# Performance work log

Hardware: AMD Instinct MI355X
Metric: run time of the kernel (lower is better)

The kernel has to match this reference:

```python
import jax, jax.numpy as jnp
import numpy as np

V, D, H, L, S, B = 32000, 512, 8, 6, 1024, 4
DH = D // H
T_ITERS = 2  # tree_iterations


def _ln(x, w, b, eps=1e-5):
    mu = jnp.mean(x, axis=-1, keepdims=True)
    var = jnp.mean((x - mu) ** 2, axis=-1, keepdims=True)
    return (x - mu) * jax.lax.rsqrt(var + eps) * w + b


def setup_inputs() -> dict:
    key = jax.random.key(0)
    ks = jax.random.split(key, 16)
    std = 0.02
    inp = {
        'input_ids': jax.random.randint(ks[0], (B, S), 0, V),
        'tok_emb': jax.random.normal(ks[1], (V, D), jnp.float32) * std,
        'pos_emb': jax.random.normal(ks[2], (S, D), jnp.float32) * std,
        # attention params, stacked over layers
        'Wq': jax.random.normal(ks[3], (L, D, D), jnp.float32) * std,
        'bq': jnp.zeros((L, D), jnp.float32),
        'Wk': jax.random.normal(ks[4], (L, D, D), jnp.float32) * std,
        'bk': jnp.zeros((L, D), jnp.float32),
        'Wv': jax.random.normal(ks[5], (L, D, D), jnp.float32) * std,
        'bv': jnp.zeros((L, D), jnp.float32),
        'Wo': jax.random.normal(ks[6], (L, D, D), jnp.float32) * std,
        'bo': jnp.zeros((L, D), jnp.float32),
        'ln1w': jnp.ones((L, D), jnp.float32), 'ln1b': jnp.zeros((L, D), jnp.float32),
        'ln2w': jnp.ones((L, D), jnp.float32), 'ln2b': jnp.zeros((L, D), jnp.float32),
        # TreeFFN params: input proj, edge proj (concat src,dst), gate
        'Win': jax.random.normal(ks[7], (L, D, D), jnp.float32) * std,
        'bin_': jnp.zeros((L, D), jnp.float32),
        'Wedge': jax.random.normal(ks[8], (L, 2 * D, D), jnp.float32) * std,
        'bedge': jnp.zeros((L, D), jnp.float32),
        'Wgate': jax.random.normal(ks[9], (L, D, D), jnp.float32) * std,
        'bgate': jnp.zeros((L, D), jnp.float32),
        'lnfw': jnp.ones((D,), jnp.float32), 'lnfb': jnp.zeros((D,), jnp.float32),
        'Whead': jax.random.normal(ks[10], (D, V), jnp.float32) * std,
    }
    return inp


def reference(input_ids, tok_emb, pos_emb, Wq, bq, Wk, bk, Wv, bv, Wo, bo,
              ln1w, ln1b, ln2w, ln2b, Win, bin_, Wedge, bedge, Wgate, bgate,
              lnfw, lnfb, Whead):
    b, s = input_ids.shape
    h = tok_emb[input_ids] + pos_emb[None, :s]  # [B,S,D]
    causal = jnp.tril(jnp.ones((s, s), bool))
    scale = 1.0 / jnp.sqrt(jnp.asarray(DH, h.dtype))
    for l in range(L):
        # --- multi-head self-attention with causal mask ---
        x = _ln(h, ln1w[l], ln1b[l])
        q = (x @ Wq[l] + bq[l]).reshape(b, s, H, DH)
        k = (x @ Wk[l] + bk[l]).reshape(b, s, H, DH)
        v = (x @ Wv[l] + bv[l]).reshape(b, s, H, DH)
        scores = jnp.einsum('bqhd,bkhd->bhqk', q, k) * scale
        scores = jnp.where(causal[None, None], scores, jnp.finfo(scores.dtype).min)
        attn = jax.nn.softmax(scores, axis=-1)
        av = jnp.einsum('bhqk,bkhd->bqhd', attn, v).reshape(b, s, D)
        h = h + av @ Wo[l] + bo[l]
        # --- TreeFFN: sequential-edge (i->i+1) message passing ---
        t = _ln(h, ln2w[l], ln2b[l]) @ Win[l] + bin_[l]
        for _ in range(T_ITERS):
            # edges: src = nodes 0..S-2, dst = nodes 1..S-1
            msg = jax.nn.relu(
                jnp.concatenate([t[:, :-1], t[:, 1:]], axis=-1) @ Wedge[l] + bedge[l]
            )  # [B,S-1,D]
            agg = jnp.pad(msg, ((0, 0), (1, 0), (0, 0)))  # scatter-add at dst nodes
            gate = jax.nn.sigmoid(agg @ Wgate[l] + bgate[l])
            t = t + gate * agg
        h = h + t
    h = _ln(h, lnfw, lnfb)
    return h @ Whead  # [B,S,V]
```

## Files before the change

### kernel.cpp

```cpp
#include <hip/hip_runtime.h>
#include <hip/hip_bf16.h>
#include <stdint.h>

#define V_ 32000
#define D_ 512
#define H_ 8
#define L_ 6
#define S_ 1024
#define B_ 4
#define DH_ 64
#define M_ (B_*S_)

typedef __attribute__((ext_vector_type(8))) short bf16x8;
typedef __attribute__((ext_vector_type(4))) short short4b;
typedef __attribute__((ext_vector_type(4))) float f32x4;

__device__ __forceinline__ short f2bs(float f) {
  union { float f; uint32_t u; } x; x.f = f;
  uint32_t r = (x.u + 0x7FFFu + ((x.u >> 16) & 1u)) >> 16;
  return (short)r;
}
__device__ __forceinline__ float bs2f(short s) {
  union { uint32_t u; float f; } x; x.u = ((uint32_t)(uint16_t)s) << 16;
  return x.f;
}

__device__ __forceinline__ f32x4 mfma16(bf16x8 a, bf16x8 b, f32x4 c) {
  return __builtin_amdgcn_mfma_f32_16x16x32_bf16(a, b, c, 0, 0, 0);
}

__device__ __forceinline__ void gload16(const short* g, char* lds) {
  __builtin_amdgcn_global_load_lds(
      (const __attribute__((address_space(1))) uint32_t*)g,
      (__attribute__((address_space(3))) uint32_t*)lds, 16, 0, 0);
}

template<int N> __device__ __forceinline__ void waitvm() {
  if constexpr (N == 0) asm volatile("s_waitcnt vmcnt(0)" ::: "memory");
  else if constexpr (N == 3) asm volatile("s_waitcnt vmcnt(3)" ::: "memory");
  else if constexpr (N == 4) asm volatile("s_waitcnt vmcnt(4)" ::: "memory");
  else if constexpr (N == 6) asm volatile("s_waitcnt vmcnt(6)" ::: "memory");
  else if constexpr (N == 8) asm volatile("s_waitcnt vmcnt(8)" ::: "memory");
}

__global__ __launch_bounds__(256) void transpose_cvt(const float* __restrict__ in,
    short* __restrict__ out, int K, int N, size_t in_slab, size_t out_slab, int orow0) {
  __shared__ float tile[32][33];
  const float* inp = in + (size_t)blockIdx.z * in_slab;
  short* outp = out + (size_t)blockIdx.z * out_slab;
  int kb = blockIdx.y * 32, nb = blockIdx.x * 32;
  int tx = threadIdx.x, ty = threadIdx.y;
  for (int r = ty; r < 32; r += 8) {
    int k = kb + r, n = nb + tx;
    tile[r][tx] = (k < K && n < N) ? inp[(size_t)k * N + n] : 0.f;
  }
  __syncthreads();
  for (int r = ty; r < 32; r += 8) {
    int n = nb + r, k = kb + tx;
    if (n < N && k < K) outp[(size_t)(orow0 + n) * K + k] = f2bs(tile[tx][r]);
  }
}

__global__ __launch_bounds__(256) void pack_qkv_bias(const float* __restrict__ bq,
    const float* __restrict__ bk, const float* __restrict__ bv, float* __restrict__ o) {
  int i = blockIdx.x * 256 + threadIdx.x;
  int l = i / 1536, c = i - l * 1536;
  float v = (c < 512) ? bq[l * 512 + c] : (c < 1024) ? bk[l * 512 + c - 512]
                                                     : bv[l * 512 + c - 1024];
  o[i] = v;
}

__global__ __launch_bounds__(256) void embed_k(const int* __restrict__ ids,
    const float* __restrict__ tok, const float* __restrict__ pos, float* __restrict__ h) {
  int bs = blockIdx.x;
  int tid = threadIdx.x;
  int s = bs & (S_ - 1);
  int id = ids[bs];
  float2 te = *(const float2*)(tok + (size_t)id * D_ + tid * 2);
  float2 pe = *(const float2*)(pos + (size_t)s * D_ + tid * 2);
  float2 r; r.x = te.x + pe.x; r.y = te.y + pe.y;
  *(float2*)(h + (size_t)bs * D_ + tid * 2) = r;
}

__global__ __launch_bounds__(256) void ln4_k(const float* __restrict__ in,
    const float* __restrict__ w, const float* __restrict__ bb, short* __restrict__ outb) {
  int wv = threadIdx.x >> 6, lane = threadIdx.x & 63;
  int row = blockIdx.x * 4 + wv;
  const float* x = in + (size_t)row * D_ + lane * 8;
  float4 v0 = *(const float4*)x;
  float4 v1 = *(const float4*)(x + 4);
  float s = v0.x + v0.y + v0.z + v0.w + v1.x + v1.y + v1.z + v1.w;
  #pragma unroll
  for (int o = 32; o; o >>= 1) s += __shfl_xor(s, o);
  float mu = s * (1.f / D_);
  float d[8] = {v0.x-mu, v0.y-mu, v0.z-mu, v0.w-mu, v1.x-mu, v1.y-mu, v1.z-mu, v1.w-mu};
  float s2 = 0.f;
  #pragma unroll
  for (int j = 0; j < 8; ++j) s2 += d[j] * d[j];
  #pragma unroll
  for (int o = 32; o; o >>= 1) s2 += __shfl_xor(s2, o);
  float rs = rsqrtf(s2 * (1.f / D_) + 1e-5f);
  float4 w0 = *(const float4*)(w + lane * 8);
  float4 w1 = *(const float4*)(w + lane * 8 + 4);
  float4 b0 = *(const float4*)(bb + lane * 8);
  float4 b1 = *(const float4*)(bb + lane * 8 + 4);
  float wj[8] = {w0.x,w0.y,w0.z,w0.w,w1.x,w1.y,w1.z,w1.w};
  float bj[8] = {b0.x,b0.y,b0.z,b0.w,b1.x,b1.y,b1.z,b1.w};
  short o8[8];
  #pragma unroll
  for (int j = 0; j < 8; ++j) o8[j] = f2bs(d[j] * rs * wj[j] + bj[j]);
  *(uint4*)(outb + (size_t)row * D_ + lane * 8) = *(uint4*)o8;
}

template<int AMODE, int EMODE, int BM, int BN>
__global__ __launch_bounds__(256) void gemm3_k(
    const short* __restrict__ A, const short* __restrict__ Wt,
    const float* __restrict__ bias, float* __restrict__ Cf,
    short* __restrict__ Cb, const short* __restrict__ Agg,
    float* __restrict__ Hf, const short* __restrict__ zpad,
    int M, int N, int K)
{
  constexpr int NF = BN / 32;
  constexpr int AR = BM / 32;
  constexpr int BR = BN / 32;
  constexpr int MI = BM / 32;
  constexpr int LOADS = AR + BR;
  __shared__ __align__(16) char As[2][BM * 128];
  __shared__ __align__(16) char Bs[2][BN * 128];
  const int tid = threadIdx.x;
  const int lane = tid & 63, w = tid >> 6;
  const int m0 = blockIdx.x * BM, n0 = blockIdx.y * BN;
  const int l15 = lane & 15, l4 = lane >> 4;
  const int wm = (w >> 1) * (BM / 2), wn = (w & 1) * (BN / 2);

  const int lrow_b = tid >> 3;
  const int kel0 = (tid & 7) * 8;
  const short* agp[AR];
  const short* agpHi[AR];
  #pragma unroll
  for (int r = 0; r < AR; ++r) {
    int lrow = r * 32 + lrow_b;
    int row = m0 + lrow;
    int kel = kel0 ^ ((lrow & 7) << 3);
    if (AMODE == 0) {
      agp[r] = A + (size_t)row * K + kel;
    } else if (AMODE == 1) {
      agp[r]   = A + (size_t)row * D_ + kel;
      agpHi[r] = ((row & (S_ - 1)) == (S_ - 1)) ? zpad + kel
                                                : A + (size_t)(row + 1) * D_ + kel;
    } else {
      agp[r] = ((row & (S_ - 1)) == 0) ? zpad + kel : A + (size_t)(row - 1) * D_ + kel;
    }
  }
  const short* bgp[BR];
  #pragma unroll
  for (int r = 0; r < BR; ++r) {
    int lrow = r * 32 + lrow_b;
    int kel = kel0 ^ ((lrow & 7) << 3);
    bgp[r] = Wt + (size_t)(n0 + lrow) * K + kel;
  }

  auto stage = [&](int buf, int k0) {
    #pragma unroll
    for (int r = 0; r < AR; ++r) {
      const short* gp;
      if (AMODE == 1) gp = (k0 < D_) ? agp[r] + k0 : agpHi[r] + (k0 - D_);
      else gp = agp[r] + k0;
      gload16(gp, As[buf] + r * 4096 + w * 1024);
    }
    #pragma unroll
    for (int r = 0; r < BR; ++r)
      gload16(bgp[r] + k0, Bs[buf] + r * 4096 + w * 1024);
  };

  const int rswz = (l15 & 7) << 4;
  int aoff[MI], boff[NF];
  #pragma unroll
  for (int i = 0; i < MI; ++i) aoff[i] = (wm + i * 16 + l15) * 128;
  #pragma unroll
  for (int j = 0; j < NF; ++j) boff[j] = (wn + j * 16 + l15) * 128;

  f32x4 acc[MI][NF] = {};

  const int nk = K >> 6;
  stage(0, 0);
  for (int t = 0; t < nk; ++t) {
    const int cur = t & 1;
    if (t + 1 < nk) { stage(cur ^ 1, (t + 1) * 64); waitvm<LOADS>(); }
    else waitvm<0>();
    __syncthreads();
    #pragma unroll
    for (int kk = 0; kk < 2; ++kk) {
      const int cb = (kk * 64 + l4 * 16) ^ rswz;
      bf16x8 af[MI], bfr[NF];
      #pragma unroll
      for (int i = 0; i < MI; ++i) af[i] = *(const bf16x8*)(As[cur] + aoff[i] + cb);
      #pragma unroll
      for (int j = 0; j < NF; ++j) bfr[j] = *(const bf16x8*)(Bs[cur] + boff[j] + cb);
      __builtin_amdgcn_s_setprio(1);
      #pragma unroll
      for (int i = 0; i < MI; ++i)
        #pragma unroll
        for (int j = 0; j < NF; ++j)
          acc[i][j] = mfma16(af[i], bfr[j], acc[i][j]);
      __builtin_amdgcn_s_setprio(0);
    }
    __syncthreads();
  }

  const int rowb = m0 + wm + l4 * 4;
  const int colb = n0 + wn + l15;
  #pragma unroll
  for (int i = 0; i < MI; ++i) {
    #pragma unroll
    for (int j = 0; j < NF; ++j) {
      int col = colb + j * 16;
      float bias_v = bias ? bias[col] : 0.f;
      #pragma unroll
      for (int r = 0; r < 4; ++r) {
        int row = rowb + i * 16 + r;
        size_t idx = (size_t)row * N + col;
        float v = acc[i][j][r] + bias_v;
        if (EMODE == 0) {
          if (Cb) { Cf[idx] = v; Cb[idx] = f2bs(v); }
          else __builtin_nontemporal_store(v, &Cf[idx]);
        } else if (EMODE == 1) {
          Cf[idx] += v;
        } else if (EMODE == 2) {
          Cb[idx] = f2bs(fmaxf(v, 0.f));
        } else if (EMODE == 3) {
          float g = 1.f / (1.f + __expf(-v));
          float aggv = ((row & (S_ - 1)) == 0) ? 0.f : bs2f(Agg[idx - N]);
          float tn = bs2f(Cb[idx]) + g * aggv;
          Cb[idx] = f2bs(tn);
        } else if (EMODE == 5) {
          float g = 1.f / (1.f + __expf(-v));
          float aggv = ((row & (S_ - 1)) == 0) ? 0.f : bs2f(Agg[idx - N]);
          Hf[idx] += bs2f(Cb[idx]) + g * aggv;
        } else if (EMODE == 6) {
          Cb[idx] = f2bs(v);
        } else {
          float sc = (col < D_) ? 0.180336880f : 1.f;
          Cb[idx] = f2bs(v * sc);
        }
      }
    }
  }
}

__global__ __launch_bounds__(256) void gemm2_k(
    const short* __restrict__ A, const short* __restrict__ Wt,
    float* __restrict__ Cf, int M, int N, int K)
{
  __shared__ __align__(16) char As[2][128 * 128];
  __shared__ __align__(16) char Bs[2][128 * 128];
  const int tid = threadIdx.x;
  const int lane = tid & 63, w = tid >> 6;
  const int nwg = gridDim.x * gridDim.y;
  const int bid = blockIdx.x + blockIdx.y * gridDim.x;
  const int swz = (bid & 7) * (nwg >> 3) + (bid >> 3);
  const int m0 = (swz % gridDim.x) * 128, n0 = (swz / gridDim.x) * 128;
  const int l15 = lane & 15, l4 = lane >> 4;
  const int wm = (w >> 1) * 64, wn = (w & 1) * 64;

  const int lrow_b = tid >> 3;
  const int kel0 = (tid & 7) * 8;
  const short* agp[4];
  const short* bgp[4];
  #pragma unroll
  for (int r = 0; r < 4; ++r) {
    int lrow = r * 32 + lrow_b;
    int kel = kel0 ^ ((lrow & 7) << 3);
    agp[r] = A + (size_t)(m0 + lrow) * K + kel;
    bgp[r] = Wt + (size_t)(n0 + lrow) * K + kel;
  }
  auto stage = [&](int buf, int k0) {
    #pragma unroll
    for (int r = 0; r < 4; ++r) gload16(agp[r] + k0, As[buf] + r * 4096 + w * 1024);
    #pragma unroll
    for (int r = 0; r < 4; ++r) gload16(bgp[r] + k0, Bs[buf] + r * 4096 + w * 1024);
  };

  const int rswz = (l15 & 7) << 4;
  int aoff[4], boff[4];
  #pragma unroll
  for (int i = 0; i < 4; ++i) aoff[i] = (wm + i * 16 + l15) * 128;
  #pragma unroll
  for (int j = 0; j < 4; ++j) boff[j] = (wn + j * 16 + l15) * 128;

  f32x4 acc[4][4] = {};
  const int nk = K >> 6;
  stage(0, 0);
  for (int t = 0; t < nk; ++t) {
    const int cur = t & 1;
    if (t + 1 < nk) { stage(cur ^ 1, (t + 1) * 64); waitvm<8>(); }
    else waitvm<0>();
    __syncthreads();
    #pragma unroll
    for (int kk = 0; kk < 2; ++kk) {
      const int cb = (kk * 64 + l4 * 16) ^ rswz;
      bf16x8 af[4], bfr[4];
      #pragma unroll
      for (int i = 0; i < 4; ++i) af[i] = *(const bf16x8*)(As[cur] + aoff[i] + cb);
      #pragma unroll
      for (int j = 0; j < 4; ++j) bfr[j] = *(const bf16x8*)(Bs[cur] + boff[j] + cb);
      __builtin_amdgcn_s_setprio(1);
      #pragma unroll
      for (int i = 0; i < 4; ++i)
        #pragma unroll
        for (int j = 0; j < 4; ++j)
          acc[i][j] = mfma16(af[i], bfr[j], acc[i][j]);
      __builtin_amdgcn_s_setprio(0);
    }
    __syncthreads();
  }

  const int rowb = m0 + wm + l4 * 4;
  const int colb = n0 + wn + l15;
  #pragma unroll
  for (int i = 0; i < 4; ++i)
    #pragma unroll
    for (int j = 0; j < 4; ++j)
      #pragma unroll
      for (int r = 0; r < 4; ++r) {
        size_t idx = (size_t)(rowb + i * 16 + r) * N + colb + j * 16;
        __builtin_nontemporal_store(acc[i][j][r], &Cf[idx]);
      }
}

__global__ __launch_bounds__(256) void fattn_k(const short* __restrict__ Qkv,
    short* __restrict__ avb)
{
  __shared__ short Ks[64][72];
  __shared__ short Vt[64][72];
  __shared__ short Pt[4][16][72];
  const int QS = 3 * D_;
  const int tid = threadIdx.x, lane = tid & 63, w = tid >> 6;
  const int bx = blockIdx.x;
  const int qt = 15 - (bx >> 5);
  const int bh = bx & 31, b = bh >> 3, hh = bh & 7;
  const int l15 = lane & 15, g = lane >> 4;

  const int qrow = qt * 64 + w * 16 + l15;
  const short* qptr = Qkv + (size_t)(b * S_ + qrow) * QS + hh * DH_;
  bf16x8 qa0 = *(const bf16x8*)(qptr + g * 8);
  bf16x8 qa1 = *(const bf16x8*)(qptr + 32 + g * 8);

  f32x4 o[4] = {};
  float mx = -1e30f, lsum = 0.f;

  auto gptr = [&](int kt, int i) {
    int c = tid + i * 256;
    int key = c >> 3, d0 = (c & 7) * 8;
    return Qkv + (size_t)(b * S_ + kt * 64 + key) * QS + hh * DH_ + d0;
  };
  uint4 kvA[2], vvA[2], kvB[2], vvB[2];
  auto load_t = [&](int kt, uint4 kv[2], uint4 vv[2]) {
    #pragma unroll
    for (int i = 0; i < 2; ++i) {
      const short* base = gptr(kt, i);
      kv[i] = *(const uint4*)(base + D_);
      vv[i] = *(const uint4*)(base + 2 * D_);
    }
  };
  auto store_t = [&](uint4 kv[2], uint4 vv[2]) {
    #pragma unroll
    for (int i = 0; i < 2; ++i) {
      int c = tid + i * 256;
      int key = c >> 3, d0 = (c & 7) * 8;
      *(uint4*)&Ks[key][d0] = kv[i];
      short vs[8]; *(uint4*)vs = vv[i];
      int a = (c & 7);
      #pragma unroll
      for (int j = 0; j < 8; ++j)
        Vt[d0 + j][key ^ (a << 3)] = vs[j];
    }
  };

  auto compute = [&](int kt) {
    const int key0 = kt * 64;
    f32x4 sc[4] = {};
    __builtin_amdgcn_s_setprio(1);
    #pragma unroll
    for (int f = 0; f < 4; ++f) {
      bf16x8 ka0 = *(const bf16x8*)&Ks[f * 16 + l15][g * 8];
      bf16x8 ka1 = *(const bf16x8*)&Ks[f * 16 + l15][32 + g * 8];
      sc[f] = mfma16(ka0, qa0, sc[f]);
      sc[f] = mfma16(ka1, qa1, sc[f]);
    }
    __builtin_amdgcn_s_setprio(0);

    float s[16];
    #pragma unroll
    for (int f = 0; f < 4; ++f)
      #pragma unroll
      for (int r = 0; r < 4; ++r)
        s[f * 4 + r] = sc[f][r];
    if (kt == qt) {
      #pragma unroll
      for (int f = 0; f < 4; ++f)
        #pragma unroll
        for (int r = 0; r < 4; ++r)
          if (key0 + f * 16 + g * 4 + r > qrow) s[f * 4 + r] = -1e30f;
    }
    float cm = s[0];
    #pragma unroll
    for (int i = 1; i < 16; ++i) cm = fmaxf(cm, s[i]);
    cm = fmaxf(cm, __shfl_xor(cm, 16));
    cm = fmaxf(cm, __shfl_xor(cm, 32));
    float mn = fmaxf(mx, cm);
    float fr = exp2f(mx - mn);
    mx = mn;
    float p[16], ss = 0.f;
    #pragma unroll
    for (int i = 0; i < 16; ++i) { p[i] = exp2f(s[i] - mn); ss += p[i]; }
    ss += __shfl_xor(ss, 16);
    ss += __shfl_xor(ss, 32);
    lsum = lsum * fr + ss;
    #pragma unroll
    for (int nt = 0; nt < 4; ++nt)
      #pragma unroll
      for (int r = 0; r < 4; ++r) o[nt][r] *= fr;

    #pragma unroll
    for (int f = 0; f < 4; ++f) {
      short tmp[4];
      #pragma unroll
      for (int r = 0; r < 4; ++r) tmp[r] = f2bs(p[f * 4 + r]);
      *(uint2*)&Pt[w][l15][f * 16 + g * 4] = *(uint2*)tmp;
    }
    __builtin_amdgcn_sched_barrier(0);
    bf16x8 pb0 = *(const bf16x8*)&Pt[w][l15][g * 8];
    bf16x8 pb1 = *(const bf16x8*)&Pt[w][l15][32 + g * 8];

    __builtin_amdgcn_s_setprio(1);
    #pragma unroll
    for (int nt = 0; nt < 4; ++nt) {
      int dim = nt * 16 + l15;
      int vswz = ((dim >> 3) & 7) << 3;
      bf16x8 va0 = *(const bf16x8*)&Vt[dim][(g * 8) ^ vswz];
      bf16x8 va1 = *(const bf16x8*)&Vt[dim][(32 + g * 8) ^ vswz];
      o[nt] = mfma16(va0, pb0, o[nt]);
      o[nt] = mfma16(va1, pb1, o[nt]);
    }
    __builtin_amdgcn_s_setprio(0);
  };

  const int ntiles = qt + 1;
  load_t(0, kvA, vvA);
  int kt = 0;
  while (true) {
    __syncthreads();
    store_t(kvA, vvA);
    if (kt + 1 < ntiles) load_t(kt + 1, kvB, vvB);
    __syncthreads();
    compute(kt);
    ++kt; if (kt >= ntiles) break;
    __syncthreads();
    store_t(kvB, vvB);
    if (kt + 1 < ntiles) load_t(kt + 1, kvA, vvA);
    __syncthreads();
    compute(kt);
    ++kt; if (kt >= ntiles) break;
  }

  const float inv = 1.f / lsum;
  #pragma unroll
  for (int nt = 0; nt < 4; ++nt) {
    short ov[4];
    #pragma unroll
    for (int r = 0; r < 4; ++r) ov[r] = f2bs(o[nt][r] * inv);
    *(short4b*)(avb + (size_t)(b * S_ + qrow) * D_ + hh * DH_ + nt * 16 + g * 4) =
        *(short4b*)ov;
  }
}

extern "C" void kernel_launch(void* const* d_in, const int* in_sizes, int n_in,
                              void* d_out, int out_size, void* d_ws, size_t ws_size,
                              hipStream_t stream) {
  const int*   ids   = (const int*)d_in[0];
  const float* tok   = (const float*)d_in[1];
  const float* pos   = (const float*)d_in[2];
  const float* Wq    = (const float*)d_in[3];
  const float* bq    = (const float*)d_in[4];
  const float* Wk    = (const float*)d_in[5];
  const float* bk    = (const float*)d_in[6];
  const float* Wv    = (const float*)d_in[7];
  const float* bv    = (const float*)d_in[8];
  const float* Wo    = (const float*)d_in[9];
  const float* bo    = (const float*)d_in[10];
  const float* ln1w  = (const float*)d_in[11];
  const float* ln1b  = (const float*)d_in[12];
  const float* ln2w  = (const float*)d_in[13];
  const float* ln2b  = (const float*)d_in[14];
  const float* Win   = (const float*)d_in[15];
  const float* bin   = (const float*)d_in[16];
  const float* Wedge = (const float*)d_in[17];
  const float* bedge = (const float*)d_in[18];
  const float* Wgate = (const float*)d_in[19];
  const float* bgate = (const float*)d_in[20];
  const float* lnfw  = (const float*)d_in[21];
  const float* lnfb  = (const float*)d_in[22];
  const float* Whead = (const float*)d_in[23];
  float* out = (float*)d_out;

  char* ws = (char*)d_ws;
  size_t off = 0;
  auto alloc = [&](size_t bytes) {
    void* p = ws + off;
    off = (off + bytes + 255) & ~(size_t)255;
    return p;
  };
  short* wqkv   = (short*)alloc((size_t)L_ * 3 * D_ * D_ * 2);
  float* bqkv   = (float*)alloc((size_t)L_ * 3 * D_ * 4);
  short* wto    = (short*)alloc((size_t)L_ * D_ * D_ * 2);
  short* wtin   = (short*)alloc((size_t)L_ * D_ * D_ * 2);
  short* wtgate = (short*)alloc((size_t)L_ * D_ * D_ * 2);
  short* wtedge = (short*)alloc((size_t)L_ * 2 * D_ * D_ * 2);
  short* wthead = (short*)alloc((size_t)V_ * D_ * 2);
  short* zpad   = (short*)alloc(4096);
  float* hbuf   = (float*)alloc((size_t)M_ * D_ * 4);
  short* xb     = (short*)alloc((size_t)M_ * D_ * 2);
  short* qkvb   = (short*)alloc((size_t)M_ * 3 * D_ * 2);
  short* avb    = (short*)alloc((size_t)M_ * D_ * 2);
  short* tbf    = (short*)alloc((size_t)M_ * D_ * 2);
  short* msgb   = (short*)alloc((size_t)M_ * D_ * 2);
  (void)ws_size; (void)in_sizes; (void)n_in; (void)out_size;

  (void)hipMemsetAsync(zpad, 0, 4096, stream);

  dim3 tblk(32, 8);
  transpose_cvt<<<dim3(16, 16, L_), tblk, 0, stream>>>(Wq, wqkv, D_, D_, (size_t)D_*D_, (size_t)3*D_*D_, 0);
  transpose_cvt<<<dim3(16, 16, L_), tblk, 0, stream>>>(Wk, wqkv, D_, D_, (size_t)D_*D_, (size_t)3*D_*D_, D_);
  transpose_cvt<<<dim3(16, 16, L_), tblk, 0, stream>>>(Wv, wqkv, D_, D_, (size_t)D_*D_, (size_t)3*D_*D_, 2*D_);
  transpose_cvt<<<dim3(16, 16, L_), tblk, 0, stream>>>(Wo, wto, D_, D_, (size_t)D_*D_, (size_t)D_*D_, 0);
  transpose_cvt<<<dim3(16, 16, L_), tblk, 0, stream>>>(Win, wtin, D_, D_, (size_t)D_*D_, (size_t)D_*D_, 0);
  transpose_cvt<<<dim3(16, 16, L_), tblk, 0, stream>>>(Wgate, wtgate, D_, D_, (size_t)D_*D_, (size_t)D_*D_, 0);
  transpose_cvt<<<dim3(16, 32, L_), tblk, 0, stream>>>(Wedge, wtedge, 2*D_, D_, (size_t)2*D_*D_, (size_t)2*D_*D_, 0);
  transpose_cvt<<<dim3(V_/32, 16, 1), tblk, 0, stream>>>(Whead, wthead, D_, V_, (size_t)D_*V_, (size_t)D_*V_, 0);
  pack_qkv_bias<<<(L_ * 3 * D_) / 256, 256, 0, stream>>>(bq, bk, bv, bqkv);

  embed_k<<<M_, 256, 0, stream>>>(ids, tok, pos, hbuf);

  dim3 g32(M_ / 32, D_ / 64);
  dim3 gqkv(M_ / 64, 3 * D_ / 128);
  for (int l = 0; l < L_; ++l) {
    size_t wofs = (size_t)l * D_ * D_;
    ln4_k<<<M_ / 4, 256, 0, stream>>>(hbuf, ln1w + l * D_, ln1b + l * D_, xb);
    gemm3_k<0,4,64,128><<<gqkv, 256, 0, stream>>>(xb, wqkv + (size_t)l * 3 * D_ * D_,
        bqkv + (size_t)l * 3 * D_, nullptr, qkvb, nullptr, nullptr, zpad, M_, 3 * D_, D_);
    fattn_k<<<B_ * H_ * (S_ / 64), 256, 0, stream>>>(qkvb, avb);
    gemm3_k<0,1,32,64><<<g32, 256, 0, stream>>>(avb, wto + wofs, bo + l * D_,
        hbuf, nullptr, nullptr, nullptr, zpad, M_, D_, D_);
    ln4_k<<<M_ / 4, 256, 0, stream>>>(hbuf, ln2w + l * D_, ln2b + l * D_, xb);
    gemm3_k<0,6,32,64><<<g32, 256, 0, stream>>>(xb, wtin + wofs, bin + l * D_,
        nullptr, tbf, nullptr, nullptr, zpad, M_, D_, D_);
    gemm3_k<1,2,32,64><<<g32, 256, 0, stream>>>(tbf, wtedge + (size_t)l * 2 * D_ * D_,
        bedge + l * D_, nullptr, msgb, nullptr, nullptr, zpad, M_, D_, 2 * D_);
    gemm3_k<2,3,32,64><<<g32, 256, 0, stream>>>(msgb, wtgate + wofs, bgate + l * D_,
        nullptr, tbf, msgb, nullptr, zpad, M_, D_, D_);
    gemm3_k<1,2,32,64><<<g32, 256, 0, stream>>>(tbf, wtedge + (size_t)l * 2 * D_ * D_,
        bedge + l * D_, nullptr, msgb, nullptr, nullptr, zpad, M_, D_, 2 * D_);
    gemm3_k<2,5,32,64><<<g32, 256, 0, stream>>>(msgb, wtgate + wofs, bgate + l * D_,
        nullptr, tbf, msgb, hbuf, zpad, M_, D_, D_);
  }
  ln4_k<<<M_ / 4, 256, 0, stream>>>(hbuf, lnfw, lnfb, xb);
  gemm2_k<<<dim3(M_ / 128, V_ / 128), 256, 0, stream>>>(xb, wthead, out, M_, V_, D_);
}
```

Baseline: 923.9 us.

## Double-buffer K/V tiles in LDS for flash attention, one barrier per tile

The attention kernel now keeps two LDS buffers for K and transposed V. Each iteration issues the global loads for the next tile, computes on the current buffer, then writes the next tile into the other buffer, so only one __syncthreads is needed per tile instead of two. The aim is to hide global-load latency behind the MFMA work and cut barrier stalls. In exchange LDS use per block roughly doubles for K/V, which may lower occupancy.

```diff
diff --git a/kernel.cpp b/kernel.cpp
--- a/kernel.cpp
+++ b/kernel.cpp
@@ -331,8 +331,8 @@
 __global__ __launch_bounds__(256) void fattn_k(const short* __restrict__ Qkv,
     short* __restrict__ avb)
 {
-  __shared__ short Ks[64][72];
-  __shared__ short Vt[64][72];
+  __shared__ short Ks[2][64][72];
+  __shared__ short Vt[2][64][72];
   __shared__ short Pt[4][16][72];
   const int QS = 3 * D_;
   const int tid = threadIdx.x, lane = tid & 63, w = tid >> 6;
@@ -363,28 +363,28 @@
       vv[i] = *(const uint4*)(base + 2 * D_);
     }
   };
-  auto store_t = [&](uint4 kv[2], uint4 vv[2]) {
+  auto store_t = [&](uint4 kv[2], uint4 vv[2], int bi) {
     #pragma unroll
     for (int i = 0; i < 2; ++i) {
       int c = tid + i * 256;
       int key = c >> 3, d0 = (c & 7) * 8;
-      *(uint4*)&Ks[key][d0] = kv[i];
+      *(uint4*)&Ks[bi][key][d0] = kv[i];
       short vs[8]; *(uint4*)vs = vv[i];
       int a = (c & 7);
       #pragma unroll
       for (int j = 0; j < 8; ++j)
-        Vt[d0 + j][key ^ (a << 3)] = vs[j];
-    }
-  };
-
-  auto compute = [&](int kt) {
+        Vt[bi][d0 + j][key ^ (a << 3)] = vs[j];
+    }
+  };
+
+  auto compute = [&](int kt, int bi) {
     const int key0 = kt * 64;
     f32x4 sc[4] = {};
     __builtin_amdgcn_s_setprio(1);
     #pragma unroll
     for (int f = 0; f < 4; ++f) {
-      bf16x8 ka0 = *(const bf16x8*)&Ks[f * 16 + l15][g * 8];
-      bf16x8 ka1 = *(const bf16x8*)&Ks[f * 16 + l15][32 + g * 8];
+      bf16x8 ka0 = *(const bf16x8*)&Ks[bi][f * 16 + l15][g * 8];
+      bf16x8 ka1 = *(const bf16x8*)&Ks[bi][f * 16 + l15][32 + g * 8];
       sc[f] = mfma16(ka0, qa0, sc[f]);
       sc[f] = mfma16(ka1, qa1, sc[f]);
     }
@@ -438,8 +438,8 @@
     for (int nt = 0; nt < 4; ++nt) {
       int dim = nt * 16 + l15;
       int vswz = ((dim >> 3) & 7) << 3;
-      bf16x8 va0 = *(const bf16x8*)&Vt[dim][(g * 8) ^ vswz];
-      bf16x8 va1 = *(const bf16x8*)&Vt[dim][(32 + g * 8) ^ vswz];
+      bf16x8 va0 = *(const bf16x8*)&Vt[bi][dim][(g * 8) ^ vswz];
+      bf16x8 va1 = *(const bf16x8*)&Vt[bi][dim][(32 + g * 8) ^ vswz];
       o[nt] = mfma16(va0, pb0, o[nt]);
       o[nt] = mfma16(va1, pb1, o[nt]);
     }
@@ -448,20 +448,23 @@
 
   const int ntiles = qt + 1;
   load_t(0, kvA, vvA);
-  int kt = 0;
+  store_t(kvA, vvA, 0);
+  __syncthreads();
+  int kt = 0, cur = 0;
   while (true) {
+    bool more = (kt + 1 < ntiles);
+    if (more) load_t(kt + 1, kvB, vvB);
+    compute(kt, cur);
+    if (more) store_t(kvB, vvB, cur ^ 1);
     __syncthreads();
-    store_t(kvA, vvA);
-    if (kt + 1 < ntiles) load_t(kt + 1, kvB, vvB);
+    ++kt; if (!more) break; cur ^= 1;
+
+    more = (kt + 1 < ntiles);
+    if (more) load_t(kt + 1, kvA, vvA);
+    compute(kt, cur);
+    if (more) store_t(kvA, vvA, cur ^ 1);
     __syncthreads();
-    compute(kt);
-    ++kt; if (kt >= ntiles) break;
-    __syncthreads();
-    store_t(kvB, vvB);
-    if (kt + 1 < ntiles) load_t(kt + 1, kvA, vvA);
-    __syncthreads();
-    compute(kt);
-    ++kt; if (kt >= ntiles) break;
+    ++kt; if (!more) break; cur ^= 1;
   }
 
   const float inv = 1.f / lsum;
```

Result: slower. 1.001 ms, median of 3 (+8.4%).
